# Optimization experiments

Hardware: AMD Instinct MI355X
Metric: run time of the kernel (lower is better)

Reference implementation:

```python
import jax, jax.numpy as jnp
import numpy as np

B, N, M = 64, 1024, 1024


def _chamfer(a, b):
    # a: [B,N,3], b: [B,M,3]; pairwise Euclidean distances via Gram trick
    d2 = (
        jnp.sum(a * a, axis=-1)[:, :, None]
        + jnp.sum(b * b, axis=-1)[:, None, :]
        - 2.0 * jnp.einsum('bnd,bmd->bnm', a, b)
    )  # [B,N,M]
    d = jnp.sqrt(jnp.maximum(d2, 0.0))
    # bidirectional nearest-neighbor distance (N == M so they align per-point slot)
    return 0.5 * (jnp.min(d, axis=2) + jnp.min(d, axis=1))  # [B,N]


def _l2(a, b):
    return jnp.linalg.norm(a - b, axis=2)  # [B,N]


def setup_inputs() -> dict:
    key = jax.random.key(0)
    k1, k2, k3, k4, k5, k6 = jax.random.split(key, 6)
    return {
        'pred_points1': jax.random.normal(k1, (B, N, 3), dtype=jnp.float32),
        'pred_points2': jax.random.normal(k2, (B, N, 3), dtype=jnp.float32),
        'target_points': jax.random.normal(k3, (B, M, 3), dtype=jnp.float32),
        'flag1': jax.random.uniform(k4, (B,), dtype=jnp.float32),
        'flag2': jax.random.uniform(k5, (B,), dtype=jnp.float32),
        'sym_flag': jax.random.uniform(k6, (B,), dtype=jnp.float32),
    }


def reference(pred_points1, pred_points2, target_points, flag1, flag2, sym_flag):
    sym_dis1 = _chamfer(pred_points1, target_points).mean(axis=1)   # [B]
    asym_dis1 = _l2(pred_points1, target_points).mean(axis=1)       # [B]
    loss1 = flag1 * (sym_flag * sym_dis1 + (1.0 - sym_flag) * asym_dis1)

    sym_dis2 = _chamfer(pred_points2, target_points).mean(axis=1)
    asym_dis2 = _l2(pred_points2, target_points).mean(axis=1)
    # flag2 multiplier makes the sum(flag2)>0 branch mathematically equivalent
    loss2 = flag2 * (sym_flag * sym_dis2 + (1.0 - sym_flag) * asym_dis2)

    all_loss = loss1 + loss2
    # (all_loss, stage1, stage2) scalar losses, stacked
    return jnp.stack([all_loss.mean(), loss1.mean(), loss2.mean()])
```

## Files before the change

### kernel.cpp

```cpp
#include <hip/hip_runtime.h>
#include <hip/hip_bf16.h>


#define BATCH 64
#define NPTS 1024

typedef __attribute__((ext_vector_type(8))) short s16x8;
typedef __attribute__((ext_vector_type(8))) unsigned short u16x8;
typedef __attribute__((ext_vector_type(16))) float f32x16;

__device__ inline unsigned short f2bf(float v) {
    __hip_bfloat16 h = __float2bfloat16(v);
    return *reinterpret_cast<unsigned short*>(&h);
}
__device__ inline float bf2f(unsigned short u) {
    __hip_bfloat16 h = *reinterpret_cast<__hip_bfloat16*>(&u);
    return __bfloat162float(h);
}

__device__ inline void pack_ab(float x, float y, float z,
                               u16x8& a0, u16x8& a1, u16x8& b0, u16x8& b1) {
    float h = fmaf(z, z, fmaf(y, y, x*x));
    unsigned short xh = f2bf(x), yh = f2bf(y), zh = f2bf(z);
    unsigned short xl = f2bf(x - bf2f(xh)), yl = f2bf(y - bf2f(yh)), zl = f2bf(z - bf2f(zh));
    float cx = -2.f*x, cy = -2.f*y, cz = -2.f*z;
    unsigned short cxh = f2bf(cx), cyh = f2bf(cy), czh = f2bf(cz);
    unsigned short cxl = f2bf(cx - bf2f(cxh)), cyl = f2bf(cy - bf2f(cyh)), czl = f2bf(cz - bf2f(czh));
    unsigned short hh = f2bf(h), hl = f2bf(h - bf2f(hh));
    const unsigned short one = 0x3F80;
    a0 = u16x8{cxh, cyh, czh, cxl, cyl, czl, cxh, cyh};
    a1 = u16x8{czh, hh, hl, one, one, 0, 0, 0};
    b0 = u16x8{xh, yh, zh, xh, yh, zh, xl, yl};
    b1 = u16x8{zl, one, one, hh, hl, 0, 0, 0};
}

__device__ inline float fold_sum(float v[16], int lane) {
    {
        const bool up = lane & 1;
        #pragma unroll
        for (int k = 0; k < 8; ++k) {
            float send = up ? v[k] : v[k+8];
            float recv = __shfl_xor(send, 1);
            v[k] = fminf(up ? v[k+8] : v[k], recv);
        }
    }
    {
        const bool up = lane & 2;
        #pragma unroll
        for (int k = 0; k < 4; ++k) {
            float send = up ? v[k] : v[k+4];
            float recv = __shfl_xor(send, 2);
            v[k] = fminf(up ? v[k+4] : v[k], recv);
        }
    }
    {
        const bool up = lane & 4;
        #pragma unroll
        for (int k = 0; k < 2; ++k) {
            float send = up ? v[k] : v[k+2];
            float recv = __shfl_xor(send, 4);
            v[k] = fminf(up ? v[k+2] : v[k], recv);
        }
    }
    {
        const bool up = lane & 8;
        float send = up ? v[0] : v[1];
        float recv = __shfl_xor(send, 8);
        v[0] = fminf(up ? v[1] : v[0], recv);
    }
    v[0] = fminf(v[0], __shfl_xor(v[0], 16));
    float d = sqrtf(fmaxf(v[0], 0.f));
    #pragma unroll
    for (int mask = 1; mask <= 32; mask <<= 1) d += __shfl_xor(d, mask);
    return d;
}

__global__ __launch_bounds__(512) void pass_kernel(
    const float* __restrict__ p1, const float* __restrict__ p2,
    const float* __restrict__ tg, float* __restrict__ ws)
{
    __shared__ __align__(16) unsigned short ybuf[16384];
    __shared__ __align__(16) unsigned short abuf[4096];
    __shared__ float red[8];
    __shared__ float redE[8];

    const int bid = blockIdx.x;
    const int j = bid >> 8, b = (bid >> 2) & 63, qt = bid & 3;
    const int tid = threadIdx.x;

    const float* __restrict__ X = (j == 0) ? p1 : (j == 1) ? p2 : tg;
    const float* __restrict__ Y = (j == 2) ? p1 : (j == 3) ? p2 : tg;

    #pragma unroll
    for (int ii = 0; ii < 2; ++ii) {
        const int i = tid + ii * 512;
        const size_t g = ((size_t)b * NPTS + i) * 3;
        float x = Y[g], y = Y[g+1], z = Y[g+2];
        u16x8 a0, a1, b0, b1;
        pack_ab(x, y, z, a0, a1, b0, b1);
        const int off = (i >> 5) * 512 + (i & 31) * 8;
        *(u16x8*)(ybuf + off)       = b0;
        *(u16x8*)(ybuf + off + 256) = b1;
    }
    float e = 0.f;
    if (tid < 256) {
        const int i = qt * 256 + tid;
        const size_t g = ((size_t)b * NPTS + i) * 3;
        float x = X[g], y = X[g+1], z = X[g+2];
        u16x8 a0, a1, b0, b1;
        pack_ab(x, y, z, a0, a1, b0, b1);
        const int off = (tid >> 5) * 512 + (tid & 31) * 8;
        *(u16x8*)(abuf + off)       = a0;
        *(u16x8*)(abuf + off + 256) = a1;
        if (j < 2) {
            float tx = tg[g], ty = tg[g+1], tz = tg[g+2];
            float dx = x - tx, dy = y - ty, dz = z - tz;
            e = sqrtf(fmaf(dz, dz, fmaf(dy, dy, dx*dx)));
        }
    }
    __syncthreads();

    const int lane = tid & 63, w = tid >> 6;
    const int c = lane & 31, q = lane >> 5;
    const int fo = q * 256 + c * 8;
    const s16x8 fa = *(const s16x8*)(abuf + w * 512 + fo);

    float rm[16];
    #pragma unroll
    for (int i = 0; i < 16; ++i) rm[i] = 3e38f;
    const f32x16 zacc = {};

    const unsigned short* Yp = ybuf + fo;
    #pragma unroll 1
    for (int t = 0; t < 32; t += 2) {
        const s16x8 bb0 = *(const s16x8*)(Yp + t * 512);
        const s16x8 bb1 = *(const s16x8*)(Yp + t * 512 + 512);
        f32x16 u0 = __builtin_amdgcn_mfma_f32_32x32x16_bf16(fa, bb0, zacc, 0, 0, 0);
        f32x16 u1 = __builtin_amdgcn_mfma_f32_32x32x16_bf16(fa, bb1, zacc, 0, 0, 0);
        #pragma unroll
        for (int i = 0; i < 16; ++i) rm[i] = fminf(rm[i], fminf(u0[i], u1[i]));
    }

    const float s = 0.5f * fold_sum(rm, lane);
    #pragma unroll
    for (int mask = 1; mask <= 32; mask <<= 1) e += __shfl_xor(e, mask);
    if (lane == 0) { red[w] = s; redE[w] = e; }
    __syncthreads();

    if (tid == 0) {
        float S = 0.f, E = 0.f;
        #pragma unroll
        for (int k = 0; k < 8; ++k) { S += red[k]; E += redE[k]; }
        ws[bid] = S;
        if (j < 2) ws[1024 + bid] = E;
    }
}

__global__ __launch_bounds__(64) void finalize_kernel(
    const float* __restrict__ flag1, const float* __restrict__ flag2,
    const float* __restrict__ symf, const float* __restrict__ ws,
    float* __restrict__ out)
{
    const int b = threadIdx.x;
    float rowS1 = 0.f, rowS2 = 0.f, colS1 = 0.f, colS2 = 0.f, E1 = 0.f, E2 = 0.f;
    #pragma unroll
    for (int qt = 0; qt < 4; ++qt) {
        rowS1 += ws[0*256 + b*4 + qt];
        rowS2 += ws[1*256 + b*4 + qt];
        colS1 += ws[2*256 + b*4 + qt];
        colS2 += ws[3*256 + b*4 + qt];
        E1    += ws[1024 + 0*256 + b*4 + qt];
        E2    += ws[1024 + 1*256 + b*4 + qt];
    }
    const float inv = 1.f / (float)NPTS;
    const float ch1 = 0.5f * (rowS1 + colS1) * inv;
    const float ch2 = 0.5f * (rowS2 + colS2) * inv;
    const float sf = symf[b];
    float l1 = flag1[b] * (sf * ch1 + (1.f - sf) * E1 * inv);
    float l2 = flag2[b] * (sf * ch2 + (1.f - sf) * E2 * inv);
    #pragma unroll
    for (int mask = 1; mask <= 32; mask <<= 1) {
        l1 += __shfl_xor(l1, mask);
        l2 += __shfl_xor(l2, mask);
    }
    if (b == 0) {
        const float s = 1.f / (float)BATCH;
        out[0] = (l1 + l2) * s;
        out[1] = l1 * s;
        out[2] = l2 * s;
    }
}

extern "C" void kernel_launch(void* const* d_in, const int* in_sizes, int n_in,
                              void* d_out, int out_size, void* d_ws, size_t ws_size,
                              hipStream_t stream) {
    const float* p1 = (const float*)d_in[0];
    const float* p2 = (const float*)d_in[1];
    const float* tg = (const float*)d_in[2];
    const float* f1 = (const float*)d_in[3];
    const float* f2 = (const float*)d_in[4];
    const float* sf = (const float*)d_in[5];
    float* out = (float*)d_out;
    float* ws = (float*)d_ws;

    pass_kernel<<<1024, 512, 0, stream>>>(p1, p2, tg, ws);
    finalize_kernel<<<1, 64, 0, stream>>>(f1, f2, sf, ws, out);
}
```

Before: 76.21 us.

## Process 512 query points per block, reusing each Y fragment for two MFMAs

Each block now handles half of a batch's query points instead of a quarter, so the grid halves and every wave computes two 32-row A tiles against each loaded B fragment. The point is to halve the per-block cost of packing the whole Y set into LDS and to reuse each LDS read of B across two MFMAs. It also replaces the bf16 conversion intrinsics with bit-truncation splitting. Truncation changes rounding of the hi part, but the lo residual still compensates. The trade-off is fewer blocks (512) for 256 CUs and more registers per wave.

```diff
diff --git a/kernel.cpp b/kernel.cpp
--- a/kernel.cpp
+++ b/kernel.cpp
@@ -9,24 +9,22 @@
 typedef __attribute__((ext_vector_type(8))) unsigned short u16x8;
 typedef __attribute__((ext_vector_type(16))) float f32x16;
 
-__device__ inline unsigned short f2bf(float v) {
-    __hip_bfloat16 h = __float2bfloat16(v);
-    return *reinterpret_cast<unsigned short*>(&h);
-}
-__device__ inline float bf2f(unsigned short u) {
-    __hip_bfloat16 h = *reinterpret_cast<__hip_bfloat16*>(&u);
-    return __bfloat162float(h);
+__device__ inline void split_bf(float v, unsigned short& hi, unsigned short& lo) {
+    unsigned int bits = __float_as_uint(v);
+    hi = (unsigned short)(bits >> 16);
+    float rec = __uint_as_float(bits & 0xFFFF0000u);
+    lo = (unsigned short)(__float_as_uint(v - rec) >> 16);
 }
 
 __device__ inline void pack_ab(float x, float y, float z,
                                u16x8& a0, u16x8& a1, u16x8& b0, u16x8& b1) {
     float h = fmaf(z, z, fmaf(y, y, x*x));
-    unsigned short xh = f2bf(x), yh = f2bf(y), zh = f2bf(z);
-    unsigned short xl = f2bf(x - bf2f(xh)), yl = f2bf(y - bf2f(yh)), zl = f2bf(z - bf2f(zh));
-    float cx = -2.f*x, cy = -2.f*y, cz = -2.f*z;
-    unsigned short cxh = f2bf(cx), cyh = f2bf(cy), czh = f2bf(cz);
-    unsigned short cxl = f2bf(cx - bf2f(cxh)), cyl = f2bf(cy - bf2f(cyh)), czl = f2bf(cz - bf2f(czh));
-    unsigned short hh = f2bf(h), hl = f2bf(h - bf2f(hh));
+    unsigned short xh, xl, yh, yl, zh, zl;
+    split_bf(x, xh, xl); split_bf(y, yh, yl); split_bf(z, zh, zl);
+    unsigned short cxh, cxl, cyh, cyl, czh, czl;
+    split_bf(-2.f*x, cxh, cxl); split_bf(-2.f*y, cyh, cyl); split_bf(-2.f*z, czh, czl);
+    unsigned short hh, hl;
+    split_bf(h, hh, hl);
     const unsigned short one = 0x3F80;
     a0 = u16x8{cxh, cyh, czh, cxl, cyl, czl, cxh, cyh};
     a1 = u16x8{czh, hh, hl, one, one, 0, 0, 0};
@@ -80,12 +78,12 @@
     const float* __restrict__ tg, float* __restrict__ ws)
 {
     __shared__ __align__(16) unsigned short ybuf[16384];
-    __shared__ __align__(16) unsigned short abuf[4096];
+    __shared__ __align__(16) unsigned short abuf[8192];
     __shared__ float red[8];
     __shared__ float redE[8];
 
     const int bid = blockIdx.x;
-    const int j = bid >> 8, b = (bid >> 2) & 63, qt = bid & 3;
+    const int j = bid >> 7, b = (bid >> 1) & 63, half = bid & 1;
     const int tid = threadIdx.x;
 
     const float* __restrict__ X = (j == 0) ? p1 : (j == 1) ? p2 : tg;
@@ -103,8 +101,8 @@
         *(u16x8*)(ybuf + off + 256) = b1;
     }
     float e = 0.f;
-    if (tid < 256) {
-        const int i = qt * 256 + tid;
+    {
+        const int i = half * 512 + tid;
         const size_t g = ((size_t)b * NPTS + i) * 3;
         float x = X[g], y = X[g+1], z = X[g+2];
         u16x8 a0, a1, b0, b1;
@@ -123,25 +121,28 @@
     const int lane = tid & 63, w = tid >> 6;
     const int c = lane & 31, q = lane >> 5;
     const int fo = q * 256 + c * 8;
-    const s16x8 fa = *(const s16x8*)(abuf + w * 512 + fo);
-
-    float rm[16];
-    #pragma unroll
-    for (int i = 0; i < 16; ++i) rm[i] = 3e38f;
+    const s16x8 fa0 = *(const s16x8*)(abuf + (2*w)   * 512 + fo);
+    const s16x8 fa1 = *(const s16x8*)(abuf + (2*w+1) * 512 + fo);
+
+    float rm0[16], rm1[16];
+    #pragma unroll
+    for (int i = 0; i < 16; ++i) { rm0[i] = 3e38f; rm1[i] = 3e38f; }
     const f32x16 zacc = {};
 
     const unsigned short* Yp = ybuf + fo;
-    #pragma unroll 1
-    for (int t = 0; t < 32; t += 2) {
-        const s16x8 bb0 = *(const s16x8*)(Yp + t * 512);
-        const s16x8 bb1 = *(const s16x8*)(Yp + t * 512 + 512);
-        f32x16 u0 = __builtin_amdgcn_mfma_f32_32x32x16_bf16(fa, bb0, zacc, 0, 0, 0);
-        f32x16 u1 = __builtin_amdgcn_mfma_f32_32x32x16_bf16(fa, bb1, zacc, 0, 0, 0);
-        #pragma unroll
-        for (int i = 0; i < 16; ++i) rm[i] = fminf(rm[i], fminf(u0[i], u1[i]));
-    }
-
-    const float s = 0.5f * fold_sum(rm, lane);
+    #pragma unroll 2
+    for (int t = 0; t < 32; ++t) {
+        const s16x8 bb = *(const s16x8*)(Yp + t * 512);
+        f32x16 u0 = __builtin_amdgcn_mfma_f32_32x32x16_bf16(fa0, bb, zacc, 0, 0, 0);
+        f32x16 u1 = __builtin_amdgcn_mfma_f32_32x32x16_bf16(fa1, bb, zacc, 0, 0, 0);
+        #pragma unroll
+        for (int i = 0; i < 16; ++i) {
+            rm0[i] = fminf(rm0[i], u0[i]);
+            rm1[i] = fminf(rm1[i], u1[i]);
+        }
+    }
+
+    const float s = 0.5f * (fold_sum(rm0, lane) + fold_sum(rm1, lane));
     #pragma unroll
     for (int mask = 1; mask <= 32; mask <<= 1) e += __shfl_xor(e, mask);
     if (lane == 0) { red[w] = s; redE[w] = e; }
@@ -152,7 +153,7 @@
         #pragma unroll
         for (int k = 0; k < 8; ++k) { S += red[k]; E += redE[k]; }
         ws[bid] = S;
-        if (j < 2) ws[1024 + bid] = E;
+        if (j < 2) ws[512 + bid] = E;
     }
 }
 
@@ -164,13 +165,13 @@
     const int b = threadIdx.x;
     float rowS1 = 0.f, rowS2 = 0.f, colS1 = 0.f, colS2 = 0.f, E1 = 0.f, E2 = 0.f;
     #pragma unroll
-    for (int qt = 0; qt < 4; ++qt) {
-        rowS1 += ws[0*256 + b*4 + qt];
-        rowS2 += ws[1*256 + b*4 + qt];
-        colS1 += ws[2*256 + b*4 + qt];
-        colS2 += ws[3*256 + b*4 + qt];
-        E1    += ws[1024 + 0*256 + b*4 + qt];
-        E2    += ws[1024 + 1*256 + b*4 + qt];
+    for (int h = 0; h < 2; ++h) {
+        rowS1 += ws[0*128 + b*2 + h];
+        rowS2 += ws[1*128 + b*2 + h];
+        colS1 += ws[2*128 + b*2 + h];
+        colS2 += ws[3*128 + b*2 + h];
+        E1    += ws[512 + 0*128 + b*2 + h];
+        E2    += ws[512 + 1*128 + b*2 + h];
     }
     const float inv = 1.f / (float)NPTS;
     const float ch1 = 0.5f * (rowS1 + colS1) * inv;
@@ -203,6 +204,6 @@
     float* out = (float*)d_out;
     float* ws = (float*)d_ws;
 
-    pass_kernel<<<1024, 512, 0, stream>>>(p1, p2, tg, ws);
+    pass_kernel<<<512, 512, 0, stream>>>(p1, p2, tg, ws);
     finalize_kernel<<<1, 64, 0, stream>>>(f1, f2, sf, ws, out);
 }
```

Result: faster. 74.04 us (-2.9%).
